# Performance work log

Measured on AMD Instinct MI355X. Metric: run time of the kernel, lower is better.

Reference implementation:

```python
import jax, jax.numpy as jnp
import numpy as np

EVENTLEN = 8  # config.event_length
NEG = -10000.0


def setup_inputs() -> dict:
    key = jax.random.key(0)
    k1, k2 = jax.random.split(key)
    T, B, E = 128, 512, 128  # decodelen, batch_size, entity_size
    feats = jax.random.normal(k1, (T, B, E), dtype=jnp.float32)
    transitions = jax.random.normal(k2, (E, E), dtype=jnp.float32)
    # Same masking the torch module applies to transitions.data at init
    transitions = transitions.at[0, :].set(NEG).at[:, -1].set(NEG)
    return {"feats": feats, "transitions": transitions}


def reference(feats, transitions):
    """Segmented CRF forward algorithm (OneCrfCCKSDecoder._forward_alg).

    feats:       [T, B, E] per-step emission scores (entity tag logits)
    transitions: [E, E]    transitions[j, k] = score of k -> j
    Returns scalar alpha / (T // EVENTLEN).
    """
    T, B, E = feats.shape
    n_events = T // EVENTLEN

    # Faithful to torch: init_alphas[:][0] = 0.0 zeroes the batch-0 ROW.
    init_fv = jnp.full((B, E), NEG, dtype=feats.dtype).at[0].set(0.0)

    t_idx = jnp.arange(T)
    is_boundary = (t_idx % EVENTLEN == 0) & (t_idx != 0)  # accumulate alpha
    is_update = (t_idx % EVENTLEN != 0)                   # DP update step

    def step(carry, inp):
        fv, alpha = carry              # fv: [B, E], alpha: scalar
        feat, bnd, upd = inp           # feat: [B, E]
        # Event-boundary accumulation (uses fv BEFORE any update; note the
        # original never resets fv inside _forward_alg).
        alpha_inc = jnp.mean(jax.nn.logsumexp(fv + transitions[-1], axis=1))
        alpha = alpha + jnp.where(bnd, alpha_inc, jnp.zeros_like(alpha_inc))
        # fv_new[b, j] = logsumexp_k( fv[b,k] + feat[b,k] + transitions[j,k] )
        x = fv + feat                                        # [B, E]
        fv_new = jax.nn.logsumexp(x[:, None, :] + transitions[None, :, :], axis=-1)
        fv = jnp.where(upd, fv_new, fv)
        return (fv, alpha), None

    (fv, alpha), _ = jax.lax.scan(
        step, (init_fv, jnp.zeros((), feats.dtype)), (feats, is_boundary, is_update)
    )
    # Terminal accumulation after the loop.
    alpha = alpha + jnp.mean(jax.nn.logsumexp(fv + transitions[-1], axis=1))
    return alpha / n_events
```

## Files before the change

kernel.cpp:

```cpp
#include <hip/hip_runtime.h>


typedef _Float16 f16x4 __attribute__((ext_vector_type(4)));
typedef _Float16 f16x8 __attribute__((ext_vector_type(8)));
typedef float    f32x4 __attribute__((ext_vector_type(4)));

#define NEG_VAL   (-10000.0f)
#define C_SCALE   0.0024787521766663585f
#define LOG_C     6.0f

#define LDS_BARRIER() asm volatile("s_waitcnt lgkmcnt(0)\n\ts_barrier" ::: "memory")

__global__ __launch_bounds__(512)
void crf_fwd(const float* __restrict__ feats,
             const float* __restrict__ trans,
             float* __restrict__ out)
{
    const int tid  = threadIdx.x;
    const int w    = tid >> 6;
    const int lane = tid & 63;
    const int bloc = lane & 15;
    const int q    = lane >> 4;
    const int b    = blockIdx.x * 16 + bloc;

    f16x8 Afrag[4];
    {
        const float* rowp = trans + (size_t)(16 * w + bloc) * 128;
        #pragma unroll
        for (int kap = 0; kap < 4; ++kap) {
            const f32x4* p = (const f32x4*)(rowp + 32 * kap + 8 * q);
            f32x4 x = p[0], y = p[1];
            f16x8 f;
            f[0] = (_Float16)__expf(x[0]); f[1] = (_Float16)__expf(x[1]);
            f[2] = (_Float16)__expf(x[2]); f[3] = (_Float16)__expf(x[3]);
            f[4] = (_Float16)__expf(y[0]); f[5] = (_Float16)__expf(y[1]);
            f[6] = (_Float16)__expf(y[2]); f[7] = (_Float16)__expf(y[3]);
            Afrag[kap] = f;
        }
    }
    f32x4 te;
    {
        f32x4 x = *(const f32x4*)(trans + 127 * 128 + 16 * w + 4 * q);
        te[0] = __expf(x[0]); te[1] = __expf(x[1]);
        te[2] = __expf(x[2]); te[3] = __expf(x[3]);
    }

    __shared__ __align__(16) char  Hbuf[4096];
    __shared__ float Spart[16 * 8];
    __shared__ float Mpart[16 * 8];

    const int waddr = bloc * 256 + (((2 * w + (q >> 1)) ^ bloc) * 16) + 8 * (q & 1);
    int raddr[4];
    #pragma unroll
    for (int kap = 0; kap < 4; ++kap)
        raddr[kap] = bloc * 256 + (((4 * kap + q) ^ bloc) * 16);

    const float* fb = feats + (size_t)b * 128 + 16 * w + 4 * q;
    f32x4 efi;
    f32x4 r1v, r2v;
    {
        f32x4 x = *(const f32x4*)(fb + 1 * 65536);
        efi[0] = __expf(x[0]) * C_SCALE; efi[1] = __expf(x[1]) * C_SCALE;
        efi[2] = __expf(x[2]) * C_SCALE; efi[3] = __expf(x[3]) * C_SCALE;
        r1v = *(const f32x4*)(fb + 2 * 65536);
        r2v = *(const f32x4*)(fb + 3 * 65536);
    }
    float logc_cur = LOG_C;

    f32x4 acc = {1.f, 1.f, 1.f, 1.f};
    float M     = (b == 0) ? 0.0f : NEG_VAL;
    float alpha = 0.0f;

    #pragma unroll 8
    for (int t = 1; t < 128; ++t) {
        const bool upd = (t & 7) != 0;
        float sc_next = C_SCALE;
        float lg_next = LOG_C;

        if (upd) {
            M += logc_cur;
            f16x4 hh;
            hh[0] = (_Float16)(acc[0] * efi[0]);
            hh[1] = (_Float16)(acc[1] * efi[1]);
            hh[2] = (_Float16)(acc[2] * efi[2]);
            hh[3] = (_Float16)(acc[3] * efi[3]);
            *(f16x4*)(Hbuf + waddr) = hh;
            LDS_BARRIER();

            f16x8 B0 = *(const f16x8*)(Hbuf + raddr[0]);
            f16x8 B1 = *(const f16x8*)(Hbuf + raddr[1]);
            f16x8 B2 = *(const f16x8*)(Hbuf + raddr[2]);
            f16x8 B3 = *(const f16x8*)(Hbuf + raddr[3]);

            f32x4 z = {0.f, 0.f, 0.f, 0.f};
            f32x4 da = __builtin_amdgcn_mfma_f32_16x16x32_f16(Afrag[0], B0, z, 0, 0, 0);
            f32x4 db = __builtin_amdgcn_mfma_f32_16x16x32_f16(Afrag[1], B1, z, 0, 0, 0);
            da = __builtin_amdgcn_mfma_f32_16x16x32_f16(Afrag[2], B2, da, 0, 0, 0);
            db = __builtin_amdgcn_mfma_f32_16x16x32_f16(Afrag[3], B3, db, 0, 0, 0);
            acc = da + db;
        } else {
            float s = acc[0] * te[0] + acc[1] * te[1]
                    + acc[2] * te[2] + acc[3] * te[3];
            float m = fmaxf(fmaxf(acc[0], acc[1]), fmaxf(acc[2], acc[3]));
            s += __shfl_xor(s, 16, 64);
            s += __shfl_xor(s, 32, 64);
            m = fmaxf(m, __shfl_xor(m, 16, 64));
            m = fmaxf(m, __shfl_xor(m, 32, 64));
            if (q == 0) {
                Spart[bloc * 8 + w] = s;
                Mpart[bloc * 8 + w] = m;
            }
            LDS_BARRIER();

            f32x4 sa = *(const f32x4*)&Spart[bloc * 8];
            f32x4 sb = *(const f32x4*)&Spart[bloc * 8 + 4];
            f32x4 ma = *(const f32x4*)&Mpart[bloc * 8];
            f32x4 mb = *(const f32x4*)&Mpart[bloc * 8 + 4];
            float r = ((sa[0] + sa[1]) + (sa[2] + sa[3]))
                    + ((sb[0] + sb[1]) + (sb[2] + sb[3]));
            float cmax = fmaxf(fmaxf(fmaxf(ma[0], ma[1]), fmaxf(ma[2], ma[3])),
                               fmaxf(fmaxf(mb[0], mb[1]), fmaxf(mb[2], mb[3])));

            alpha += M + __logf(r);
            sc_next = C_SCALE * __builtin_amdgcn_rcpf(cmax);
            lg_next = LOG_C + __logf(cmax);
        }

        if (t + 1 < 128) {
            efi[0] = __expf(r1v[0]) * sc_next; efi[1] = __expf(r1v[1]) * sc_next;
            efi[2] = __expf(r1v[2]) * sc_next; efi[3] = __expf(r1v[3]) * sc_next;
            logc_cur = lg_next;
            r1v = r2v;
            if (t + 3 < 128) r2v = *(const f32x4*)(fb + (size_t)(t + 3) * 65536);
        }
    }

    {
        float s = acc[0] * te[0] + acc[1] * te[1]
                + acc[2] * te[2] + acc[3] * te[3];
        s += __shfl_xor(s, 16, 64);
        s += __shfl_xor(s, 32, 64);
        if (q == 0) Spart[bloc * 8 + w] = s;
        LDS_BARRIER();
        f32x4 sa = *(const f32x4*)&Spart[bloc * 8];
        f32x4 sb = *(const f32x4*)&Spart[bloc * 8 + 4];
        float r = ((sa[0] + sa[1]) + (sa[2] + sa[3]))
                + ((sb[0] + sb[1]) + (sb[2] + sb[3]));
        alpha += M + __logf(r);
    }

    if (w == 0) {
        float v = alpha;
        #pragma unroll
        for (int off = 1; off < 64; off <<= 1)
            v += __shfl_xor(v, off, 64);
        if (lane == 0)
            atomicAdd(out, v * (1.0f / (4.0f * 512.0f * 16.0f)));
    }
}

extern "C" void kernel_launch(void* const* d_in, const int* in_sizes, int n_in,
                              void* d_out, int out_size, void* d_ws, size_t ws_size,
                              hipStream_t stream) {
    const float* feats = (const float*)d_in[0];
    const float* trans = (const float*)d_in[1];
    float* out = (float*)d_out;

    hipMemsetAsync(out, 0, sizeof(float), stream);
    crf_fwd<<<32, 512, 0, stream>>>(feats, trans, out);
}
```

Before: 113.2 us.

## Halve workgroup to four waves, each computing two output row tiles

```diff
diff --git a/kernel.cpp b/kernel.cpp
--- a/kernel.cpp
+++ b/kernel.cpp
@@ -11,7 +11,7 @@
 
 #define LDS_BARRIER() asm volatile("s_waitcnt lgkmcnt(0)\n\ts_barrier" ::: "memory")
 
-__global__ __launch_bounds__(512)
+__global__ __launch_bounds__(256)
 void crf_fwd(const float* __restrict__ feats,
              const float* __restrict__ trans,
              float* __restrict__ out)
@@ -23,9 +23,10 @@
     const int q    = lane >> 4;
     const int b    = blockIdx.x * 16 + bloc;
 
-    f16x8 Afrag[4];
-    {
-        const float* rowp = trans + (size_t)(16 * w + bloc) * 128;
+    f16x8 Afrag[2][4];
+    #pragma unroll
+    for (int tile = 0; tile < 2; ++tile) {
+        const float* rowp = trans + (size_t)(16 * (2 * w + tile) + bloc) * 128;
         #pragma unroll
         for (int kap = 0; kap < 4; ++kap) {
             const f32x4* p = (const f32x4*)(rowp + 32 * kap + 8 * q);
@@ -35,39 +36,50 @@
             f[2] = (_Float16)__expf(x[2]); f[3] = (_Float16)__expf(x[3]);
             f[4] = (_Float16)__expf(y[0]); f[5] = (_Float16)__expf(y[1]);
             f[6] = (_Float16)__expf(y[2]); f[7] = (_Float16)__expf(y[3]);
-            Afrag[kap] = f;
+            Afrag[tile][kap] = f;
         }
     }
-    f32x4 te;
+    f32x4 te0, te1;
     {
-        f32x4 x = *(const f32x4*)(trans + 127 * 128 + 16 * w + 4 * q);
-        te[0] = __expf(x[0]); te[1] = __expf(x[1]);
-        te[2] = __expf(x[2]); te[3] = __expf(x[3]);
+        f32x4 x = *(const f32x4*)(trans + 127 * 128 + 16 * (2 * w + 0) + 4 * q);
+        te0[0] = __expf(x[0]); te0[1] = __expf(x[1]);
+        te0[2] = __expf(x[2]); te0[3] = __expf(x[3]);
+        f32x4 y = *(const f32x4*)(trans + 127 * 128 + 16 * (2 * w + 1) + 4 * q);
+        te1[0] = __expf(y[0]); te1[1] = __expf(y[1]);
+        te1[2] = __expf(y[2]); te1[3] = __expf(y[3]);
     }
 
     __shared__ __align__(16) char  Hbuf[4096];
-    __shared__ float Spart[16 * 8];
-    __shared__ float Mpart[16 * 8];
+    __shared__ float Spart[16 * 4];
+    __shared__ float Mpart[16 * 4];
 
-    const int waddr = bloc * 256 + (((2 * w + (q >> 1)) ^ bloc) * 16) + 8 * (q & 1);
+    const int waddr0 = bloc * 256 + (((4 * w + 0 + (q >> 1)) ^ bloc) * 16) + 8 * (q & 1);
+    const int waddr1 = bloc * 256 + (((4 * w + 2 + (q >> 1)) ^ bloc) * 16) + 8 * (q & 1);
     int raddr[4];
     #pragma unroll
     for (int kap = 0; kap < 4; ++kap)
         raddr[kap] = bloc * 256 + (((4 * kap + q) ^ bloc) * 16);
 
-    const float* fb = feats + (size_t)b * 128 + 16 * w + 4 * q;
-    f32x4 efi;
-    f32x4 r1v, r2v;
+    const float* fb0 = feats + (size_t)b * 128 + 32 * w + 4 * q;
+    const float* fb1 = fb0 + 16;
+    f32x4 efi0, efi1;
+    f32x4 r1v0, r1v1, r2v0, r2v1;
     {
-        f32x4 x = *(const f32x4*)(fb + 1 * 65536);
-        efi[0] = __expf(x[0]) * C_SCALE; efi[1] = __expf(x[1]) * C_SCALE;
-        efi[2] = __expf(x[2]) * C_SCALE; efi[3] = __expf(x[3]) * C_SCALE;
-        r1v = *(const f32x4*)(fb + 2 * 65536);
-        r2v = *(const f32x4*)(fb + 3 * 65536);
+        f32x4 x = *(const f32x4*)(fb0 + 1 * 65536);
+        f32x4 y = *(const f32x4*)(fb1 + 1 * 65536);
+        efi0[0] = __expf(x[0]) * C_SCALE; efi0[1] = __expf(x[1]) * C_SCALE;
+        efi0[2] = __expf(x[2]) * C_SCALE; efi0[3] = __expf(x[3]) * C_SCALE;
+        efi1[0] = __expf(y[0]) * C_SCALE; efi1[1] = __expf(y[1]) * C_SCALE;
+        efi1[2] = __expf(y[2]) * C_SCALE; efi1[3] = __expf(y[3]) * C_SCALE;
+        r1v0 = *(const f32x4*)(fb0 + 2 * 65536);
+        r1v1 = *(const f32x4*)(fb1 + 2 * 65536);
+        r2v0 = *(const f32x4*)(fb0 + 3 * 65536);
+        r2v1 = *(const f32x4*)(fb1 + 3 * 65536);
     }
     float logc_cur = LOG_C;
 
-    f32x4 acc = {1.f, 1.f, 1.f, 1.f};
+    f32x4 acc0 = {1.f, 1.f, 1.f, 1.f};
+    f32x4 acc1 = {1.f, 1.f, 1.f, 1.f};
     float M     = (b == 0) ? 0.0f : NEG_VAL;
     float alpha = 0.0f;
 
@@ -79,12 +91,17 @@
 
         if (upd) {
             M += logc_cur;
-            f16x4 hh;
-            hh[0] = (_Float16)(acc[0] * efi[0]);
-            hh[1] = (_Float16)(acc[1] * efi[1]);
-            hh[2] = (_Float16)(acc[2] * efi[2]);
-            hh[3] = (_Float16)(acc[3] * efi[3]);
-            *(f16x4*)(Hbuf + waddr) = hh;
+            f16x4 h0, h1;
+            h0[0] = (_Float16)(acc0[0] * efi0[0]);
+            h0[1] = (_Float16)(acc0[1] * efi0[1]);
+            h0[2] = (_Float16)(acc0[2] * efi0[2]);
+            h0[3] = (_Float16)(acc0[3] * efi0[3]);
+            h1[0] = (_Float16)(acc1[0] * efi1[0]);
+            h1[1] = (_Float16)(acc1[1] * efi1[1]);
+            h1[2] = (_Float16)(acc1[2] * efi1[2]);
+            h1[3] = (_Float16)(acc1[3] * efi1[3]);
+            *(f16x4*)(Hbuf + waddr0) = h0;
+            *(f16x4*)(Hbuf + waddr1) = h1;
             LDS_BARRIER();
 
             f16x8 B0 = *(const f16x8*)(Hbuf + raddr[0]);
@@ -93,33 +110,37 @@
             f16x8 B3 = *(const f16x8*)(Hbuf + raddr[3]);
 
             f32x4 z = {0.f, 0.f, 0.f, 0.f};
-            f32x4 da = __builtin_amdgcn_mfma_f32_16x16x32_f16(Afrag[0], B0, z, 0, 0, 0);
-            f32x4 db = __builtin_amdgcn_mfma_f32_16x16x32_f16(Afrag[1], B1, z, 0, 0, 0);
-            da = __builtin_amdgcn_mfma_f32_16x16x32_f16(Afrag[2], B2, da, 0, 0, 0);
-            db = __builtin_amdgcn_mfma_f32_16x16x32_f16(Afrag[3], B3, db, 0, 0, 0);
-            acc = da + db;
+            f32x4 da0 = __builtin_amdgcn_mfma_f32_16x16x32_f16(Afrag[0][0], B0, z, 0, 0, 0);
+            f32x4 db0 = __builtin_amdgcn_mfma_f32_16x16x32_f16(Afrag[0][1], B1, z, 0, 0, 0);
+            f32x4 da1 = __builtin_amdgcn_mfma_f32_16x16x32_f16(Afrag[1][0], B0, z, 0, 0, 0);
+            f32x4 db1 = __builtin_amdgcn_mfma_f32_16x16x32_f16(Afrag[1][1], B1, z, 0, 0, 0);
+            da0 = __builtin_amdgcn_mfma_f32_16x16x32_f16(Afrag[0][2], B2, da0, 0, 0, 0);
+            db0 = __builtin_amdgcn_mfma_f32_16x16x32_f16(Afrag[0][3], B3, db0, 0, 0, 0);
+            da1 = __builtin_amdgcn_mfma_f32_16x16x32_f16(Afrag[1][2], B2, da1, 0, 0, 0);
+            db1 = __builtin_amdgcn_mfma_f32_16x16x32_f16(Afrag[1][3], B3, db1, 0, 0, 0);
+            acc0 = da0 + db0;
+            acc1 = da1 + db1;
         } else {
-            float s = acc[0] * te[0] + acc[1] * te[1]
-                    + acc[2] * te[2] + acc[3] * te[3];
-            float m = fmaxf(fmaxf(acc[0], acc[1]), fmaxf(acc[2], acc[3]));
+            float s = acc0[0] * te0[0] + acc0[1] * te0[1]
+                    + acc0[2] * te0[2] + acc0[3] * te0[3]
+                    + acc1[0] * te1[0] + acc1[1] * te1[1]
+                    + acc1[2] * te1[2] + acc1[3] * te1[3];
+            float m = fmaxf(fmaxf(fmaxf(acc0[0], acc0[1]), fmaxf(acc0[2], acc0[3])),
+                            fmaxf(fmaxf(acc1[0], acc1[1]), fmaxf(acc1[2], acc1[3])));
             s += __shfl_xor(s, 16, 64);
             s += __shfl_xor(s, 32, 64);
             m = fmaxf(m, __shfl_xor(m, 16, 64));
             m = fmaxf(m, __shfl_xor(m, 32, 64));
             if (q == 0) {
-                Spart[bloc * 8 + w] = s;
-                Mpart[bloc * 8 + w] = m;
+                Spart[bloc * 4 + w] = s;
+                Mpart[bloc * 4 + w] = m;
             }
             LDS_BARRIER();
 
-            f32x4 sa = *(const f32x4*)&Spart[bloc * 8];
-            f32x4 sb = *(const f32x4*)&Spart[bloc * 8 + 4];
-            f32x4 ma = *(const f32x4*)&Mpart[bloc * 8];
-            f32x4 mb = *(const f32x4*)&Mpart[bloc * 8 + 4];
-            float r = ((sa[0] + sa[1]) + (sa[2] + sa[3]))
-                    + ((sb[0] + sb[1]) + (sb[2] + sb[3]));
-            float cmax = fmaxf(fmaxf(fmaxf(ma[0], ma[1]), fmaxf(ma[2], ma[3])),
-                               fmaxf(fmaxf(mb[0], mb[1]), fmaxf(mb[2], mb[3])));
+            f32x4 sa = *(const f32x4*)&Spart[bloc * 4];
+            f32x4 ma = *(const f32x4*)&Mpart[bloc * 4];
+            float r    = (sa[0] + sa[1]) + (sa[2] + sa[3]);
+            float cmax = fmaxf(fmaxf(ma[0], ma[1]), fmaxf(ma[2], ma[3]));
 
             alpha += M + __logf(r);
             sc_next = C_SCALE * __builtin_amdgcn_rcpf(cmax);
@@ -127,25 +148,30 @@
         }
 
         if (t + 1 < 128) {
-            efi[0] = __expf(r1v[0]) * sc_next; efi[1] = __expf(r1v[1]) * sc_next;
-            efi[2] = __expf(r1v[2]) * sc_next; efi[3] = __expf(r1v[3]) * sc_next;
+            efi0[0] = __expf(r1v0[0]) * sc_next; efi0[1] = __expf(r1v0[1]) * sc_next;
+            efi0[2] = __expf(r1v0[2]) * sc_next; efi0[3] = __expf(r1v0[3]) * sc_next;
+            efi1[0] = __expf(r1v1[0]) * sc_next; efi1[1] = __expf(r1v1[1]) * sc_next;
+            efi1[2] = __expf(r1v1[2]) * sc_next; efi1[3] = __expf(r1v1[3]) * sc_next;
             logc_cur = lg_next;
-            r1v = r2v;
-            if (t + 3 < 128) r2v = *(const f32x4*)(fb + (size_t)(t + 3) * 65536);
+            r1v0 = r2v0; r1v1 = r2v1;
+            if (t + 3 < 128) {
+                r2v0 = *(const f32x4*)(fb0 + (size_t)(t + 3) * 65536);
+                r2v1 = *(const f32x4*)(fb1 + (size_t)(t + 3) * 65536);
+            }
         }
     }
 
     {
-        float s = acc[0] * te[0] + acc[1] * te[1]
-                + acc[2] * te[2] + acc[3] * te[3];
+        float s = acc0[0] * te0[0] + acc0[1] * te0[1]
+                + acc0[2] * te0[2] + acc0[3] * te0[3]
+                + acc1[0] * te1[0] + acc1[1] * te1[1]
+                + acc1[2] * te1[2] + acc1[3] * te1[3];
         s += __shfl_xor(s, 16, 64);
         s += __shfl_xor(s, 32, 64);
-        if (q == 0) Spart[bloc * 8 + w] = s;
+        if (q == 0) Spart[bloc * 4 + w] = s;
         LDS_BARRIER();
-        f32x4 sa = *(const f32x4*)&Spart[bloc * 8];
-        f32x4 sb = *(const f32x4*)&Spart[bloc * 8 + 4];
-        float r = ((sa[0] + sa[1]) + (sa[2] + sa[3]))
-                + ((sb[0] + sb[1]) + (sb[2] + sb[3]));
+        f32x4 sa = *(const f32x4*)&Spart[bloc * 4];
+        float r = (sa[0] + sa[1]) + (sa[2] + sa[3]);
         alpha += M + __logf(r);
     }
 
@@ -167,5 +193,5 @@
     float* out = (float*)d_out;
 
     hipMemsetAsync(out, 0, sizeof(float), stream);
-    crf_fwd<<<32, 512, 0, stream>>>(feats, trans, out);
+    crf_fwd<<<32, 256, 0, stream>>>(feats, trans, out);
 }
```

Result: slower. 124.9 us (+10.3%).
